# Optimization experiments

Measured on AMD Instinct MI355X. Metric: run time of the kernel, lower is better.

Reference implementation:

```python
import jax, jax.numpy as jnp
import numpy as np

B, S, D = 8, 2048, 1024

def setup_inputs() -> dict:
    key = jax.random.key(0)
    k1, k2, k3, k4, k5, k6 = jax.random.split(key, 6)
    scale = 1.0 / np.sqrt(D)
    return {
        "input": jax.random.normal(k1, (B, S, D), dtype=jnp.float32),
        "context": jax.random.normal(k2, (B, S, D), dtype=jnp.float32),
        "Wq": jax.random.normal(k3, (D, D), dtype=jnp.float32) * scale,
        "Wk": jax.random.normal(k4, (D, D), dtype=jnp.float32) * scale,
        "Wv": jax.random.normal(k5, (D, D), dtype=jnp.float32) * scale,
        "Wo": jax.random.normal(k6, (D, D), dtype=jnp.float32) * scale,
    }

def reference(input, context, Wq, Wk, Wv, Wo):
    # Linear projections (bias-free); torch Linear stores weight as [out, in],
    # here Wq etc. are [in, out] used directly as x @ W.
    q = jnp.einsum('bsd,de->bse', input, Wq)    # [B, Sq, E]
    k = jnp.einsum('bsd,de->bse', context, Wk)  # [B, Sk, E]
    v = jnp.einsum('bsd,de->bse', context, Wv)  # [B, Sk, E]
    inv_sqrt_d = 1.0 / jnp.sqrt(jnp.asarray(k.shape[-1], dtype=q.dtype))
    scores = jnp.einsum('bqe,bke->bqk', q, k) * inv_sqrt_d  # [B, Sq, Sk]
    weights = jax.nn.softmax(scores, axis=-1)
    ctx = jnp.einsum('bqk,bke->bqe', weights, v)            # [B, Sq, E]
    # dropout layers are identity in eval/inference mode
    output = jnp.einsum('bqe,ef->bqf', ctx, Wo)             # [B, Sq, E]
    return (output, weights)
```

## Files before the change

kernel.cpp:

```cpp
#include <hip/hip_runtime.h>
#include <hip/hip_bf16.h>
#include <stdint.h>


typedef __bf16 bf16;
typedef __attribute__((ext_vector_type(8))) __bf16 bf16x8;
typedef __attribute__((ext_vector_type(4))) float f32x4;

#define BM 128
#define BN 128
#define BK 32

__device__ __forceinline__ void g2lds16(const void* g, void* l) {
    __builtin_amdgcn_global_load_lds(
        (__attribute__((address_space(1))) void*)g,
        (__attribute__((address_space(3))) void*)l,
        16, 0, 0);
}

template <bool BF16OUT>
__global__ __launch_bounds__(256) void gemm_bt(
    const bf16* __restrict__ A, const bf16* __restrict__ Bt, void* __restrict__ Cv,
    int K, int lda, int ldb, int ldc,
    long sA, long sB, long sC, float scale,
    int gx, int gy, int rowsPerXcd)
{
    __shared__ bf16 As[BM * BK];
    __shared__ bf16 Bs[BN * BK];

    const int gid  = blockIdx.x;
    const int xcd  = gid & 7;
    const int slot = gid >> 3;
    const int tx   = slot % gx;
    const int row  = xcd * rowsPerXcd + slot / gx;
    const int ty   = row % gy;
    const int z    = row / gy;

    A  += (long)z * sA;
    Bt += (long)z * sB;

    const int t    = threadIdx.x;
    const int wave = t >> 6, lane = t & 63;
    const int wr   = wave >> 1, wc = wave & 1;
    const int lm   = lane & 15, lk = lane >> 4;

    const long by = (long)ty * BM;
    const long bx = (long)tx * BN;

    f32x4 acc[4][4] = {};

    const int srow = t >> 2;
    const int scol = (t & 3) * 8;
    const bf16* Ap = A  + (by + srow) * (long)lda + scol;
    const bf16* Bp = Bt + (bx + srow) * (long)ldb + scol;
    bf16* AsW = &As[t * 8];
    bf16* BsW = &Bs[t * 8];
    const long a64 = 64L * lda, b64 = 64L * ldb;

    for (int kt = 0; kt < K; kt += BK) {
        g2lds16(Ap,       AsW);
        g2lds16(Ap + a64, AsW + 64 * BK);
        g2lds16(Bp,       BsW);
        g2lds16(Bp + b64, BsW + 64 * BK);
        Ap += BK; Bp += BK;
        __builtin_amdgcn_s_waitcnt(0x0f70);
        __syncthreads();

        bf16x8 af[4], bfr[4];
        #pragma unroll
        for (int i = 0; i < 4; ++i)
            af[i] = *(const bf16x8*)&As[(wr * 64 + i * 16 + lm) * BK + lk * 8];
        #pragma unroll
        for (int j = 0; j < 4; ++j)
            bfr[j] = *(const bf16x8*)&Bs[(wc * 64 + j * 16 + lm) * BK + lk * 8];

        #pragma unroll
        for (int i = 0; i < 4; ++i)
            #pragma unroll
            for (int j = 0; j < 4; ++j)
                acc[i][j] = __builtin_amdgcn_mfma_f32_16x16x32_bf16(
                    af[i], bfr[j], acc[i][j], 0, 0, 0);
        __syncthreads();
    }

    const long r0b = by + wr * 64 + lk * 4;
    const long c0b = bx + wc * 64 + lm;
    if (BF16OUT) {
        bf16* C = (bf16*)Cv + (long)z * sC;
        #pragma unroll
        for (int i = 0; i < 4; ++i) {
            const long rb = r0b + i * 16;
            #pragma unroll
            for (int j = 0; j < 4; ++j) {
                const long cc = c0b + j * 16;
                #pragma unroll
                for (int r = 0; r < 4; ++r)
                    C[(rb + r) * (long)ldc + cc] = (bf16)(acc[i][j][r] * scale);
            }
        }
    } else {
        float* C = (float*)Cv + (long)z * sC;
        #pragma unroll
        for (int i = 0; i < 4; ++i) {
            const long rb = r0b + i * 16;
            #pragma unroll
            for (int j = 0; j < 4; ++j) {
                const long cc = c0b + j * 16;
                #pragma unroll
                for (int r = 0; r < 4; ++r)
                    C[(rb + r) * (long)ldc + cc] = acc[i][j][r] * scale;
            }
        }
    }
}

__global__ __launch_bounds__(256) void f32_to_bf16_k(
    const float* __restrict__ in, bf16* __restrict__ out, long n)
{
    long i = ((long)blockIdx.x * blockDim.x + threadIdx.x) * 8;
    if (i + 8 > n) return;
    const float4* p = (const float4*)(in + i);
    float4 a = p[0], b = p[1];
    bf16x8 o = { (bf16)a.x, (bf16)a.y, (bf16)a.z, (bf16)a.w,
                 (bf16)b.x, (bf16)b.y, (bf16)b.z, (bf16)b.w };
    *(bf16x8*)(out + i) = o;
}

template <typename Tin>
__global__ __launch_bounds__(256) void transpose_to_bf16(
    const Tin* __restrict__ in, bf16* __restrict__ out,
    int R, int C, long sIn, long sOut)
{
    __shared__ bf16 tile[32][33];
    in  += (long)blockIdx.z * sIn;
    out += (long)blockIdx.z * sOut;
    const int bx = blockIdx.x * 32, by = blockIdx.y * 32;
    const int tx = threadIdx.x, ty = threadIdx.y;
    #pragma unroll
    for (int r = ty; r < 32; r += 8)
        tile[r][tx] = (bf16)in[(long)(by + r) * C + bx + tx];
    __syncthreads();
    #pragma unroll
    for (int r = ty; r < 32; r += 8)
        out[(long)(bx + r) * R + by + tx] = tile[tx][r];
}

__global__ __launch_bounds__(256) void softmax_rows(
    float* __restrict__ sc, bf16* __restrict__ wbf, int n)
{
    const long base = (long)blockIdx.x * n;
    const int t = threadIdx.x;
    const int wave = t >> 6, lane = t & 63;
    float v[8];
    #pragma unroll
    for (int k = 0; k < 8; ++k) v[k] = sc[base + t + k * 256];

    float m = v[0];
    #pragma unroll
    for (int k = 1; k < 8; ++k) m = fmaxf(m, v[k]);
    #pragma unroll
    for (int off = 32; off; off >>= 1) m = fmaxf(m, __shfl_xor(m, off, 64));
    __shared__ float red[4];
    if (lane == 0) red[wave] = m;
    __syncthreads();
    m = fmaxf(fmaxf(red[0], red[1]), fmaxf(red[2], red[3]));

    float s = 0.f;
    #pragma unroll
    for (int k = 0; k < 8; ++k) { v[k] = __expf(v[k] - m); s += v[k]; }
    #pragma unroll
    for (int off = 32; off; off >>= 1) s += __shfl_xor(s, off, 64);
    __syncthreads();
    if (lane == 0) red[wave] = s;
    __syncthreads();
    s = red[0] + red[1] + red[2] + red[3];
    const float inv = 1.0f / s;
    #pragma unroll
    for (int k = 0; k < 8; ++k) {
        float w = v[k] * inv;
        sc[base + t + k * 256]  = w;
        wbf[base + t + k * 256] = (bf16)w;
    }
}

extern "C" void kernel_launch(void* const* d_in, const int* in_sizes, int n_in,
                              void* d_out, int out_size, void* d_ws, size_t ws_size,
                              hipStream_t stream)
{
    const int Bb = 8, S = 2048, D = 1024;
    const long BSD = (long)Bb * S * D;
    const long DD  = (long)D * D;

    const float* input   = (const float*)d_in[0];
    const float* context = (const float*)d_in[1];
    const float* Wq = (const float*)d_in[2];
    const float* Wk = (const float*)d_in[3];
    const float* Wv = (const float*)d_in[4];
    const float* Wo = (const float*)d_in[5];

    bf16* Xbf = (bf16*)d_ws;
    bf16* Cbf = Xbf + BSD;
    bf16* Kbf = Cbf + BSD;
    bf16* Qbf = Kbf + BSD;
    bf16* VT  = Qbf + BSD;
    bf16* WqT = VT + BSD;
    bf16* WkT = WqT + DD;
    bf16* WvT = WkT + DD;
    bf16* WoT = WvT + DD;
    bf16* ctxb = Xbf;
    bf16* Wbf  = Cbf;

    float* outp   = (float*)d_out;
    float* scores = outp + BSD;

    const dim3 blk256(256);
    const dim3 tb(32, 8);

    f32_to_bf16_k<<<dim3((unsigned)(BSD / 8 / 256)), blk256, 0, stream>>>(input,   Xbf, BSD);
    f32_to_bf16_k<<<dim3((unsigned)(BSD / 8 / 256)), blk256, 0, stream>>>(context, Cbf, BSD);

    transpose_to_bf16<float><<<dim3(32, 32, 1), tb, 0, stream>>>(Wq, WqT, D, D, 0, 0);
    transpose_to_bf16<float><<<dim3(32, 32, 1), tb, 0, stream>>>(Wk, WkT, D, D, 0, 0);
    transpose_to_bf16<float><<<dim3(32, 32, 1), tb, 0, stream>>>(Wv, WvT, D, D, 0, 0);
    transpose_to_bf16<float><<<dim3(32, 32, 1), tb, 0, stream>>>(Wo, WoT, D, D, 0, 0);

    gemm_bt<true><<<dim3(1024), blk256, 0, stream>>>(
        Xbf, WqT, Qbf, D, D, D, D, 0, 0, 0, 1.0f, 8, 128, 16);
    gemm_bt<true><<<dim3(1024), blk256, 0, stream>>>(
        Cbf, WkT, Kbf, D, D, D, D, 0, 0, 0, 1.0f, 8, 128, 16);
    gemm_bt<true><<<dim3(1024), blk256, 0, stream>>>(
        WvT, Cbf, VT, D, D, D, S, 0, (long)S * D, (long)D * S, 1.0f, 16, 8, 8);

    gemm_bt<false><<<dim3(2048), blk256, 0, stream>>>(
        Qbf, Kbf, scores, D, D, D, S,
        (long)S * D, (long)S * D, (long)S * S, 0.03125f, 16, 16, 16);

    softmax_rows<<<dim3(Bb * S), blk256, 0, stream>>>(scores, Wbf, S);

    gemm_bt<true><<<dim3(1024), blk256, 0, stream>>>(
        Wbf, VT, ctxb, S, S, S, D,
        (long)S * S, (long)D * S, (long)S * D, 1.0f, 8, 16, 16);

    gemm_bt<false><<<dim3(1024), blk256, 0, stream>>>(
        ctxb, WoT, outp, D, D, D, D, 0, 0, 0, 1.0f, 8, 128, 16);
}
```

Before: 787.2 us.

## Rewrite GEMM as 256x256 tile, 8-wave, double-buffered LDS pipeline with swizzle

Replaces the 128x128x32 single-buffered GEMM with a 256x256x64 tile computed by 8 waves. The kernel uses 128KB of dynamic LDS, double-buffered and filled by split async global-to-LDS loads that overlap the MFMA work. It also adds an XOR swizzle against LDS bank conflicts, s_setprio around the MFMA blocks, and finer-grained barriers. The aim is more data reuse per tile and hidden load latency, at the cost of one block per CU and fewer blocks overall, which may cause tail imbalance.

Result: faster. 650.6 us (-17.4%).

```diff
diff --git a/kernel.cpp b/kernel.cpp
--- a/kernel.cpp
+++ b/kernel.cpp
@@ -6,10 +6,6 @@
 typedef __bf16 bf16;
 typedef __attribute__((ext_vector_type(8))) __bf16 bf16x8;
 typedef __attribute__((ext_vector_type(4))) float f32x4;
-
-#define BM 128
-#define BN 128
-#define BK 32
 
 __device__ __forceinline__ void g2lds16(const void* g, void* l) {
     __builtin_amdgcn_global_load_lds(
@@ -18,81 +14,183 @@
         16, 0, 0);
 }
 
+#define ABUF(p) ((p) * 32768)
+#define BBUF(p) (65536 + (p) * 32768)
+
+__device__ __forceinline__ void stage_chunk(
+    const bf16* __restrict__ gsrc, int ld, char* ldsbuf, int c,
+    int tr, int colElem, int t)
+{
+    g2lds16(gsrc + (long)(c * 64 + tr) * ld + colElem,
+            ldsbuf + c * 8192 + t * 16);
+}
+
 template <bool BF16OUT>
-__global__ __launch_bounds__(256) void gemm_bt(
+__global__ __launch_bounds__(512) void gemm_bt(
     const bf16* __restrict__ A, const bf16* __restrict__ Bt, void* __restrict__ Cv,
     int K, int lda, int ldb, int ldc,
     long sA, long sB, long sC, float scale,
     int gx, int gy, int rowsPerXcd)
 {
-    __shared__ bf16 As[BM * BK];
-    __shared__ bf16 Bs[BN * BK];
+    extern __shared__ __align__(16) char lds[];
 
     const int gid  = blockIdx.x;
     const int xcd  = gid & 7;
     const int slot = gid >> 3;
     const int tx   = slot % gx;
-    const int row  = xcd * rowsPerXcd + slot / gx;
-    const int ty   = row % gy;
-    const int z    = row / gy;
+    const int rw   = xcd * rowsPerXcd + slot / gx;
+    const int ty   = rw % gy;
+    const int z    = rw / gy;
 
     A  += (long)z * sA;
     Bt += (long)z * sB;
 
-    const int t    = threadIdx.x;
-    const int wave = t >> 6, lane = t & 63;
-    const int wr   = wave >> 1, wc = wave & 1;
-    const int lm   = lane & 15, lk = lane >> 4;
-
-    const long by = (long)ty * BM;
-    const long bx = (long)tx * BN;
-
-    f32x4 acc[4][4] = {};
-
-    const int srow = t >> 2;
-    const int scol = (t & 3) * 8;
-    const bf16* Ap = A  + (by + srow) * (long)lda + scol;
-    const bf16* Bp = Bt + (bx + srow) * (long)ldb + scol;
-    bf16* AsW = &As[t * 8];
-    bf16* BsW = &Bs[t * 8];
-    const long a64 = 64L * lda, b64 = 64L * ldb;
-
-    for (int kt = 0; kt < K; kt += BK) {
-        g2lds16(Ap,       AsW);
-        g2lds16(Ap + a64, AsW + 64 * BK);
-        g2lds16(Bp,       BsW);
-        g2lds16(Bp + b64, BsW + 64 * BK);
-        Ap += BK; Bp += BK;
-        __builtin_amdgcn_s_waitcnt(0x0f70);
-        __syncthreads();
-
+    const int t  = threadIdx.x;
+    const int wv = t >> 6, lane = t & 63;
+    const int wm = wv >> 2, wn = wv & 3;
+    const int lm = lane & 15, lk = lane >> 4;
+
+    const long by = (long)ty * 256;
+    const long bx = (long)tx * 256;
+
+    const bf16* Ab = A  + by * (long)lda;
+    const bf16* Bb = Bt + bx * (long)ldb;
+
+    const int tr      = t >> 3;
+    const int colElem = ((t & 7) * 8) ^ (((t >> 5) & 1) * 16);
+
+    const int lkx   = (lk * 16) ^ ((lm & 4) << 3);
+    const int aOff0 = (wm * 128 + lm) * 128 + lkx;
+    const int bOff0 = (wn * 64  + lm) * 128 + lkx;
+
+    f32x4 acc[8][4] = {};
+    const int NT = K >> 6;
+
+    stage_chunk(Ab, lda, lds + ABUF(0), 0, tr, colElem, t);
+    stage_chunk(Ab, lda, lds + ABUF(0), 2, tr, colElem, t);
+    stage_chunk(Bb, ldb, lds + BBUF(0), 0, tr, colElem, t);
+    stage_chunk(Bb, ldb, lds + BBUF(0), 1, tr, colElem, t);
+    stage_chunk(Bb, ldb, lds + BBUF(0), 2, tr, colElem, t);
+    stage_chunk(Bb, ldb, lds + BBUF(0), 3, tr, colElem, t);
+    stage_chunk(Ab, lda, lds + ABUF(0), 1, tr, colElem, t);
+    stage_chunk(Ab, lda, lds + ABUF(0), 3, tr, colElem, t);
+    if (NT > 1) {
+        stage_chunk(Ab + 64, lda, lds + ABUF(1), 0, tr, colElem, t);
+        stage_chunk(Ab + 64, lda, lds + ABUF(1), 2, tr, colElem, t);
+        stage_chunk(Bb + 64, ldb, lds + BBUF(1), 0, tr, colElem, t);
+        stage_chunk(Bb + 64, ldb, lds + BBUF(1), 1, tr, colElem, t);
+    }
+
+    for (int u = 0; u < NT; ++u) {
+        char* aC = lds + ABUF(u & 1);
+        char* bC = lds + BBUF(u & 1);
         bf16x8 af[4], bfr[4];
-        #pragma unroll
-        for (int i = 0; i < 4; ++i)
-            af[i] = *(const bf16x8*)&As[(wr * 64 + i * 16 + lm) * BK + lk * 8];
+
+        if (u + 1 < NT) {
+            const bf16* An = Ab + (u + 1) * 64;
+            const bf16* Bn = Bb + (u + 1) * 64;
+            char* aN = lds + ABUF((u + 1) & 1);
+            char* bN = lds + BBUF((u + 1) & 1);
+            stage_chunk(Bn, ldb, bN, 2, tr, colElem, t);
+            stage_chunk(Bn, ldb, bN, 3, tr, colElem, t);
+            stage_chunk(An, lda, aN, 1, tr, colElem, t);
+            stage_chunk(An, lda, aN, 3, tr, colElem, t);
+            asm volatile("s_waitcnt vmcnt(8)" ::: "memory");
+        } else {
+            asm volatile("s_waitcnt vmcnt(0)" ::: "memory");
+        }
+        __builtin_amdgcn_s_barrier();
+        asm volatile("" ::: "memory");
+
+        #pragma unroll
+        for (int i = 0; i < 4; ++i)
+            af[i] = *(const bf16x8*)(aC + aOff0 + i * 2048);
         #pragma unroll
         for (int j = 0; j < 4; ++j)
-            bfr[j] = *(const bf16x8*)&Bs[(wc * 64 + j * 16 + lm) * BK + lk * 8];
-
+            bfr[j] = *(const bf16x8*)(bC + bOff0 + j * 2048);
+        asm volatile("s_waitcnt lgkmcnt(0)" ::: "memory");
+        __builtin_amdgcn_s_setprio(1);
         #pragma unroll
         for (int i = 0; i < 4; ++i)
             #pragma unroll
             for (int j = 0; j < 4; ++j)
                 acc[i][j] = __builtin_amdgcn_mfma_f32_16x16x32_bf16(
                     af[i], bfr[j], acc[i][j], 0, 0, 0);
-        __syncthreads();
-    }
-
-    const long r0b = by + wr * 64 + lk * 4;
-    const long c0b = bx + wc * 64 + lm;
+        __builtin_amdgcn_s_setprio(0);
+        asm volatile("" ::: "memory");
+        __builtin_amdgcn_s_barrier();
+        asm volatile("" ::: "memory");
+
+        #pragma unroll
+        for (int i = 0; i < 4; ++i)
+            af[i] = *(const bf16x8*)(aC + aOff0 + (i + 4) * 2048);
+        asm volatile("s_waitcnt lgkmcnt(0)" ::: "memory");
+        __builtin_amdgcn_s_setprio(1);
+        #pragma unroll
+        for (int i = 0; i < 4; ++i)
+            #pragma unroll
+            for (int j = 0; j < 4; ++j)
+                acc[i + 4][j] = __builtin_amdgcn_mfma_f32_16x16x32_bf16(
+                    af[i], bfr[j], acc[i + 4][j], 0, 0, 0);
+        __builtin_amdgcn_s_setprio(0);
+        asm volatile("" ::: "memory");
+        __builtin_amdgcn_s_barrier();
+        asm volatile("" ::: "memory");
+
+        #pragma unroll
+        for (int i = 0; i < 4; ++i)
+            af[i] = *(const bf16x8*)(aC + aOff0 + i * 2048 + 64);
+        #pragma unroll
+        for (int j = 0; j < 4; ++j)
+            bfr[j] = *(const bf16x8*)(bC + bOff0 + j * 2048 + 64);
+        asm volatile("s_waitcnt lgkmcnt(0)" ::: "memory");
+        __builtin_amdgcn_s_setprio(1);
+        #pragma unroll
+        for (int i = 0; i < 4; ++i)
+            #pragma unroll
+            for (int j = 0; j < 4; ++j)
+                acc[i][j] = __builtin_amdgcn_mfma_f32_16x16x32_bf16(
+                    af[i], bfr[j], acc[i][j], 0, 0, 0);
+        __builtin_amdgcn_s_setprio(0);
+        asm volatile("" ::: "memory");
+        __builtin_amdgcn_s_barrier();
+        asm volatile("" ::: "memory");
+
+        #pragma unroll
+        for (int i = 0; i < 4; ++i)
+            af[i] = *(const bf16x8*)(aC + aOff0 + (i + 4) * 2048 + 64);
+        if (u + 2 < NT) {
+            const bf16* An = Ab + (u + 2) * 64;
+            const bf16* Bn = Bb + (u + 2) * 64;
+            stage_chunk(An, lda, aC, 0, tr, colElem, t);
+            stage_chunk(An, lda, aC, 2, tr, colElem, t);
+            stage_chunk(Bn, ldb, bC, 0, tr, colElem, t);
+            stage_chunk(Bn, ldb, bC, 1, tr, colElem, t);
+        }
+        asm volatile("s_waitcnt lgkmcnt(0)" ::: "memory");
+        __builtin_amdgcn_s_setprio(1);
+        #pragma unroll
+        for (int i = 0; i < 4; ++i)
+            #pragma unroll
+            for (int j = 0; j < 4; ++j)
+                acc[i + 4][j] = __builtin_amdgcn_mfma_f32_16x16x32_bf16(
+                    af[i], bfr[j], acc[i + 4][j], 0, 0, 0);
+        __builtin_amdgcn_s_setprio(0);
+        asm volatile("" ::: "memory");
+        __builtin_amdgcn_s_barrier();
+        asm volatile("" ::: "memory");
+    }
+
+    const long r0 = by + wm * 128 + lk * 4;
+    const long c0 = bx + wn * 64 + lm;
     if (BF16OUT) {
         bf16* C = (bf16*)Cv + (long)z * sC;
         #pragma unroll
-        for (int i = 0; i < 4; ++i) {
-            const long rb = r0b + i * 16;
+        for (int i = 0; i < 8; ++i) {
+            const long rb = r0 + i * 16;
             #pragma unroll
             for (int j = 0; j < 4; ++j) {
-                const long cc = c0b + j * 16;
+                const long cc = c0 + j * 16;
                 #pragma unroll
                 for (int r = 0; r < 4; ++r)
                     C[(rb + r) * (long)ldc + cc] = (bf16)(acc[i][j][r] * scale);
@@ -101,11 +199,11 @@
     } else {
         float* C = (float*)Cv + (long)z * sC;
         #pragma unroll
-        for (int i = 0; i < 4; ++i) {
-            const long rb = r0b + i * 16;
+        for (int i = 0; i < 8; ++i) {
+            const long rb = r0 + i * 16;
             #pragma unroll
             for (int j = 0; j < 4; ++j) {
-                const long cc = c0b + j * 16;
+                const long cc = c0 + j * 16;
                 #pragma unroll
                 for (int r = 0; r < 4; ++r)
                     C[(rb + r) * (long)ldc + cc] = acc[i][j][r] * scale;
@@ -214,7 +312,18 @@
     float* scores = outp + BSD;
 
     const dim3 blk256(256);
+    const dim3 blk512(512);
     const dim3 tb(32, 8);
+    const int LDSZ = 131072;
+
+    static bool attrDone = false;
+    if (!attrDone) {
+        hipFuncSetAttribute((const void*)gemm_bt<true>,
+                            hipFuncAttributeMaxDynamicSharedMemorySize, LDSZ);
+        hipFuncSetAttribute((const void*)gemm_bt<false>,
+                            hipFuncAttributeMaxDynamicSharedMemorySize, LDSZ);
+        attrDone = true;
+    }
 
     f32_to_bf16_k<<<dim3((unsigned)(BSD / 8 / 256)), blk256, 0, stream>>>(input,   Xbf, BSD);
     f32_to_bf16_k<<<dim3((unsigned)(BSD / 8 / 256)), blk256, 0, stream>>>(context, Cbf, BSD);
@@ -224,23 +333,23 @@
     transpose_to_bf16<float><<<dim3(32, 32, 1), tb, 0, stream>>>(Wv, WvT, D, D, 0, 0);
     transpose_to_bf16<float><<<dim3(32, 32, 1), tb, 0, stream>>>(Wo, WoT, D, D, 0, 0);
 
-    gemm_bt<true><<<dim3(1024), blk256, 0, stream>>>(
-        Xbf, WqT, Qbf, D, D, D, D, 0, 0, 0, 1.0f, 8, 128, 16);
-    gemm_bt<true><<<dim3(1024), blk256, 0, stream>>>(
-        Cbf, WkT, Kbf, D, D, D, D, 0, 0, 0, 1.0f, 8, 128, 16);
-    gemm_bt<true><<<dim3(1024), blk256, 0, stream>>>(
-        WvT, Cbf, VT, D, D, D, S, 0, (long)S * D, (long)D * S, 1.0f, 16, 8, 8);
-
-    gemm_bt<false><<<dim3(2048), blk256, 0, stream>>>(
+    gemm_bt<true><<<dim3(256), blk512, LDSZ, stream>>>(
+        Xbf, WqT, Qbf, D, D, D, D, 0, 0, 0, 1.0f, 4, 64, 8);
+    gemm_bt<true><<<dim3(256), blk512, LDSZ, stream>>>(
+        Cbf, WkT, Kbf, D, D, D, D, 0, 0, 0, 1.0f, 4, 64, 8);
+    gemm_bt<true><<<dim3(256), blk512, LDSZ, stream>>>(
+        WvT, Cbf, VT, D, D, D, S, 0, (long)S * D, (long)D * S, 1.0f, 8, 4, 4);
+
+    gemm_bt<false><<<dim3(512), blk512, LDSZ, stream>>>(
         Qbf, Kbf, scores, D, D, D, S,
-        (long)S * D, (long)S * D, (long)S * S, 0.03125f, 16, 16, 16);
+        (long)S * D, (long)S * D, (long)S * S, 0.03125f, 8, 8, 8);
 
     softmax_rows<<<dim3(Bb * S), blk256, 0, stream>>>(scores, Wbf, S);
 
-    gemm_bt<true><<<dim3(1024), blk256, 0, stream>>>(
+    gemm_bt<true><<<dim3(256), blk512, LDSZ, stream>>>(
         Wbf, VT, ctxb, S, S, S, D,
-        (long)S * S, (long)D * S, (long)S * D, 1.0f, 8, 16, 16);
-
-    gemm_bt<false><<<dim3(1024), blk256, 0, stream>>>(
-        ctxb, WoT, outp, D, D, D, D, 0, 0, 0, 1.0f, 8, 128, 16);
-}
+        (long)S * S, (long)D * S, (long)S * D, 1.0f, 4, 8, 8);
+
+    gemm_bt<false><<<dim3(256), blk512, LDSZ, stream>>>(
+        ctxb, WoT, outp, D, D, D, D, 0, 0, 0, 1.0f, 4, 64, 8);
+}
```
